# Kernel optimization log

Hardware: AMD Instinct MI355X
Metric: run time of the kernel (lower is better)

## Reference

```python
import jax, jax.numpy as jnp
import numpy as np

B = 2048          # batch of tree nodes
C = 256           # num_classes (GRU input size)
HS = 512          # h_size
H2 = 2 * HS       # GRU hidden size
D = 8             # max_output_degree


def setup_inputs() -> dict:
    key = jax.random.key(0)
    ks = jax.random.split(key, 12)
    s_ih = 1.0 / np.sqrt(C)
    s_h = 1.0 / np.sqrt(H2)
    return {
        "parent_output_label": jax.random.uniform(ks[0], (B, C), dtype=jnp.float32),
        "parent_h": jax.random.normal(ks[1], (B, HS), dtype=jnp.float32),
        "encoding": jax.random.normal(ks[2], (B, HS), dtype=jnp.float32),
        # stacked GRUCell params over the D output-degree slots
        "W_ih": jax.random.uniform(ks[3], (D, 3 * H2, C), jnp.float32, -s_ih, s_ih),
        "W_hh": jax.random.uniform(ks[4], (D, 3 * H2, H2), jnp.float32, -s_h, s_h),
        "b_ih": jax.random.uniform(ks[5], (D, 3 * H2), jnp.float32, -s_h, s_h),
        "b_hh": jax.random.uniform(ks[6], (D, 3 * H2), jnp.float32, -s_h, s_h),
        # stacked linear_probs (2h -> 1) and linear_hiddens (2h -> h)
        "W_p": jax.random.uniform(ks[7], (D, H2), jnp.float32, -s_h, s_h),
        "b_p": jax.random.uniform(ks[8], (D,), jnp.float32, -s_h, s_h),
        "W_h": jax.random.uniform(ks[9], (D, HS, H2), jnp.float32, -s_h, s_h),
        "b_h": jax.random.uniform(ks[10], (D, HS), jnp.float32, -s_h, s_h),
    }


def _compute_state_probs(x, h0, W_ih, W_hh, b_ih, b_hh, W_p, b_p, W_h, b_h):
    # x: [B, C], h0: [B, H2]. All D GRUCells fused into batched einsums.
    gi = jnp.einsum("bc,dgc->bdg", x, W_ih) + b_ih[None]        # [B, D, 3*H2]
    gh = jnp.einsum("bh,dgh->bdg", h0, W_hh) + b_hh[None]       # [B, D, 3*H2]
    i_r, i_z, i_n = jnp.split(gi, 3, axis=-1)
    h_r, h_z, h_n = jnp.split(gh, 3, axis=-1)
    r = jax.nn.sigmoid(i_r + h_r)
    z = jax.nn.sigmoid(i_z + h_z)
    n = jnp.tanh(i_n + r * h_n)
    hn = (1.0 - z) * n + z * h0[:, None, :]                      # [B, D, H2]
    probs = jax.nn.sigmoid(jnp.einsum("bdh,dh->bd", hn, W_p) + b_p[None])  # [B, D]
    hc = jnp.einsum("bdh,dkh->bdk", hn, W_h) + b_h[None]         # [B, D, HS]
    h = jnp.tanh(jnp.sum(hc, axis=1))                            # activ over summed slot hiddens
    return h, probs


def reference(parent_output_label, parent_h, encoding,
              W_ih, W_hh, b_ih, b_hh, W_p, b_p, W_h, b_h):
    h0 = jnp.concatenate([parent_h, encoding], axis=1)           # [B, 2*h_size]
    return _compute_state_probs(parent_output_label, h0,
                                W_ih, W_hh, b_ih, b_hh, W_p, b_p, W_h, b_h)
```

## Files before the change

### kernel.cpp

```cpp
#include <hip/hip_runtime.h>


#define B_   2048
#define C_   256
#define HS_  512
#define H2_  1024
#define G3_  3072
#define D_   8
#define NG_  24576

typedef __attribute__((ext_vector_type(8))) short bfrag;
typedef __attribute__((ext_vector_type(4))) float f32x4;

static __device__ __forceinline__ unsigned short f2bf(float f) {
  unsigned u = __float_as_uint(f);
  u = (u + 0x7FFFu + ((u >> 16) & 1u)) >> 16;
  return (unsigned short)u;
}
static __device__ __forceinline__ float bf2f(unsigned short s) {
  return __uint_as_float(((unsigned)s) << 16);
}
static __device__ __forceinline__ float fast_sigmoid(float x) {
  return 1.f / (1.f + __expf(-x));
}
static __device__ __forceinline__ float fast_tanh(float x) {
  return 1.f - 2.f / (__expf(2.f * x) + 1.f);
}

__device__ __forceinline__ void load16(const void* g, void* l) {
  __builtin_amdgcn_global_load_lds((const __attribute__((address_space(1))) void*)g,
                                   (__attribute__((address_space(3))) void*)l,
                                   16, 0, 0);
}

__global__ __launch_bounds__(256) void pack_kernel(
    const float* __restrict__ x, const float* __restrict__ ph,
    const float* __restrict__ enc, const float* __restrict__ Wih,
    const float* __restrict__ Whh, const float* __restrict__ Wh,
    unsigned short* __restrict__ A1, unsigned short* __restrict__ A2,
    unsigned short* __restrict__ BWih, unsigned short* __restrict__ BWhh,
    unsigned short* __restrict__ BWh)
{
  const long long total4 = 38273024LL / 4;
  const long long stride = (long long)gridDim.x * blockDim.x;
  for (long long i = (long long)blockIdx.x * blockDim.x + threadIdx.x;
       i < total4; i += stride) {
    long long o = i * 4;
    float4 v;
    unsigned short* dst;
    if (o < 524288) {
      v = *(const float4*)(x + o);
      dst = A1 + o;
    } else if (o < 2621440) {
      long long rel = o - 524288;
      int b = (int)(rel >> 10), c = (int)(rel & 1023);
      const float* src = (c < 512) ? (ph + b * 512 + c) : (enc + b * 512 + (c - 512));
      v = *(const float4*)src;
      dst = A2 + rel;
    } else if (o < 8912896) {
      long long rel = o - 2621440;
      v = *(const float4*)(Wih + rel);
      dst = BWih + rel;
    } else if (o < 34078720) {
      long long rel = o - 8912896;
      v = *(const float4*)(Whh + rel);
      dst = BWhh + rel;
    } else {
      long long rel = o - 34078720;
      int kk = (int)(rel >> 13);
      int r2 = (int)(rel & 8191);
      int d = r2 >> 10, hh = r2 & 1023;
      v = *(const float4*)(Wh + ((long long)d * 524288 + kk * 1024 + hh));
      dst = BWh + rel;
    }
    ushort4 w;
    w.x = f2bf(v.x); w.y = f2bf(v.y); w.z = f2bf(v.z); w.w = f2bf(v.w);
    *(ushort4*)dst = w;
  }
}

__global__ __launch_bounds__(512, 2) void gemm256(
    const unsigned short* __restrict__ A, const unsigned short* __restrict__ Bt,
    unsigned short* __restrict__ out, int M, int N, int K)
{
  extern __shared__ char lds[];
  const int t = threadIdx.x;
  const int wave = t >> 6, lane = t & 63;
  const int wr = wave >> 2, wc = wave & 3;
  const int la = lane & 15, ls = lane >> 4;

  const int gridY = M >> 8;
  const int q8 = gridDim.x >> 3;
  const int orig = blockIdx.x;
  const int swz = (orig & 7) * q8 + (orig >> 3);
  const int by = swz % gridY;
  const int bx = swz / gridY;
  const int brow = by << 8, bcol = bx << 8;
  const int nT = K >> 6;

  const int srr = t >> 3;
  const int ssc = ((t & 7) ^ ((t >> 3) & 7)) << 3;

  auto stageA = [&](int kt, int buf, int hf) {
    const unsigned short* src = A + (size_t)(brow + hf * 128 + srr) * K + kt * 64 + ssc;
    char* dst = lds + buf * 32768 + hf * 16384 + t * 16;
    load16(src, dst);
    load16(src + (size_t)64 * K, dst + 8192);
  };
  auto stageB = [&](int kt, int buf, int hf) {
    const unsigned short* src = Bt + (size_t)(bcol + hf * 128 + srr) * K + kt * 64 + ssc;
    char* dst = lds + 65536 + buf * 32768 + hf * 16384 + t * 16;
    load16(src, dst);
    load16(src + (size_t)64 * K, dst + 8192);
  };

  const int t1 = (nT > 1) ? 1 : 0;
  stageA(0, 0, 0); stageA(0, 0, 1);
  stageB(0, 0, 0); stageB(0, 0, 1);
  stageA(t1, 1, 0); stageA(t1, 1, 1);
  asm volatile("s_waitcnt vmcnt(4)" ::: "memory");
  __builtin_amdgcn_s_barrier();

  f32x4 acc[8][4];
#pragma unroll
  for (int m = 0; m < 8; ++m)
#pragma unroll
    for (int n = 0; n < 4; ++n) acc[m][n] = (f32x4){0.f, 0.f, 0.f, 0.f};

  const int sw = (la & 7) << 4;
  const int c0 = (ls << 4) ^ sw;

  for (int kt = 0; kt < nT; ++kt) {
    const int buf = kt & 1;
    const int kt1 = (kt + 1 < nT) ? kt + 1 : nT - 1;
    const int kt2 = (kt + 2 < nT) ? kt + 2 : nT - 1;
    const char* ab = lds + buf * 32768 + wr * 16384;
    const char* bb = lds + 65536 + buf * 32768 + (wc >> 1) * 16384;
    const int brb = (wc & 1) * 64;
    bfrag a0[8], a1[8], b0[4], b1[4];

#pragma unroll
    for (int m = 0; m < 8; ++m)
      a0[m] = *(const bfrag*)(ab + (m * 16 + la) * 128 + c0);
#pragma unroll
    for (int n = 0; n < 4; ++n)
      b0[n] = *(const bfrag*)(bb + (brb + n * 16 + la) * 128 + c0);
    stageB(kt1, buf ^ 1, 0);
    __builtin_amdgcn_s_barrier();
    __builtin_amdgcn_s_setprio(1);
#pragma unroll
    for (int m = 0; m < 4; ++m)
#pragma unroll
      for (int n = 0; n < 4; ++n)
        acc[m][n] = __builtin_amdgcn_mfma_f32_16x16x32_bf16(a0[m], b0[n], acc[m][n], 0, 0, 0);
    __builtin_amdgcn_s_setprio(0);
    __builtin_amdgcn_s_barrier();

#pragma unroll
    for (int m = 0; m < 8; ++m)
      a1[m] = *(const bfrag*)(ab + (m * 16 + la) * 128 + (c0 ^ 64));
    stageB(kt1, buf ^ 1, 1);
    __builtin_amdgcn_s_barrier();
    __builtin_amdgcn_s_setprio(1);
#pragma unroll
    for (int m = 4; m < 8; ++m)
#pragma unroll
      for (int n = 0; n < 4; ++n)
        acc[m][n] = __builtin_amdgcn_mfma_f32_16x16x32_bf16(a0[m], b0[n], acc[m][n], 0, 0, 0);
    __builtin_amdgcn_s_setprio(0);
    asm volatile("s_waitcnt lgkmcnt(0)" ::: "memory");
    __builtin_amdgcn_s_barrier();

#pragma unroll
    for (int n = 0; n < 4; ++n)
      b1[n] = *(const bfrag*)(bb + (brb + n * 16 + la) * 128 + (c0 ^ 64));
    stageA(kt2, buf, 0);
    __builtin_amdgcn_s_barrier();
    __builtin_amdgcn_s_setprio(1);
#pragma unroll
    for (int m = 0; m < 4; ++m)
#pragma unroll
      for (int n = 0; n < 4; ++n)
        acc[m][n] = __builtin_amdgcn_mfma_f32_16x16x32_bf16(a1[m], b1[n], acc[m][n], 0, 0, 0);
    __builtin_amdgcn_s_setprio(0);
    __builtin_amdgcn_s_barrier();

    stageA(kt2, buf, 1);
    __builtin_amdgcn_s_barrier();
    __builtin_amdgcn_s_setprio(1);
#pragma unroll
    for (int m = 4; m < 8; ++m)
#pragma unroll
      for (int n = 0; n < 4; ++n)
        acc[m][n] = __builtin_amdgcn_mfma_f32_16x16x32_bf16(a1[m], b1[n], acc[m][n], 0, 0, 0);
    __builtin_amdgcn_s_setprio(0);
    asm volatile("s_waitcnt vmcnt(4)" ::: "memory");
    __builtin_amdgcn_s_barrier();
  }

  const int orow = brow + wr * 128 + ls * 4;
  const int ocol = bcol + wc * 64 + la;
#pragma unroll
  for (int m = 0; m < 8; ++m)
#pragma unroll
    for (int n = 0; n < 4; ++n)
#pragma unroll
      for (int r = 0; r < 4; ++r)
        out[(size_t)(orow + m * 16 + r) * N + (ocol + n * 16)] = f2bf(acc[m][n][r]);
}

__global__ __launch_bounds__(256) void gemm_bt(
    const unsigned short* __restrict__ A, const unsigned short* __restrict__ Bt,
    void* __restrict__ out, int M, int N, int K, int kPerSlice, int outF32)
{
  __shared__ unsigned short sA[128 * 32];
  __shared__ unsigned short sB[128 * 32];
  const int t = threadIdx.x;
  const int wave = t >> 6, lane = t & 63;
  const int wr = wave >> 1, wc = wave & 1;
  const int brow = blockIdx.y << 7;
  const int bcol = blockIdx.x << 7;
  const int kOff = blockIdx.z * kPerSlice;

  f32x4 acc[4][4];
#pragma unroll
  for (int m = 0; m < 4; m++)
#pragma unroll
    for (int n = 0; n < 4; n++) acc[m][n] = (f32x4){0.f, 0.f, 0.f, 0.f};

  const int srow = t >> 2;
  const int scol = (t & 3) << 3;
  const unsigned short* aSrc = A + (size_t)(brow + srow) * K + kOff + scol;
  const unsigned short* bSrc = Bt + (size_t)(bcol + srow) * K + kOff + scol;
  const size_t rowStep = (size_t)64 * K;
  unsigned short* dA0 = sA + wave * 512;
  unsigned short* dA1 = sA + 2048 + wave * 512;
  unsigned short* dB0 = sB + wave * 512;
  unsigned short* dB1 = sB + 2048 + wave * 512;

  const int la = lane & 15;
  const int lk = (lane >> 4) << 3;
  const int kSteps = kPerSlice >> 5;

  for (int ks = 0; ks < kSteps; ++ks) {
    load16(aSrc, dA0);
    load16(aSrc + rowStep, dA1);
    load16(bSrc, dB0);
    load16(bSrc + rowStep, dB1);
    aSrc += 32; bSrc += 32;
    __syncthreads();
    bfrag aF[4], bF[4];
#pragma unroll
    for (int m = 0; m < 4; m++)
      aF[m] = *(const bfrag*)&sA[(wr * 64 + m * 16 + la) * 32 + lk];
#pragma unroll
    for (int n = 0; n < 4; n++)
      bF[n] = *(const bfrag*)&sB[(wc * 64 + n * 16 + la) * 32 + lk];
#pragma unroll
    for (int m = 0; m < 4; m++)
#pragma unroll
      for (int n = 0; n < 4; n++)
        acc[m][n] = __builtin_amdgcn_mfma_f32_16x16x32_bf16(aF[m], bF[n], acc[m][n], 0, 0, 0);
    __syncthreads();
  }

  const int orow = brow + wr * 64 + (lane >> 4) * 4;
  const int ocol = bcol + wc * 64 + la;
  if (outF32) {
    float* o = (float*)out + (size_t)blockIdx.z * ((size_t)M * N);
#pragma unroll
    for (int m = 0; m < 4; m++) {
      const int rb = orow + m * 16;
#pragma unroll
      for (int n = 0; n < 4; n++) {
        const int cb = ocol + n * 16;
#pragma unroll
        for (int r = 0; r < 4; r++)
          o[(size_t)(rb + r) * N + cb] = acc[m][n][r];
      }
    }
  } else {
    unsigned short* o = (unsigned short*)out;
#pragma unroll
    for (int m = 0; m < 4; m++) {
      const int rb = orow + m * 16;
#pragma unroll
      for (int n = 0; n < 4; n++) {
        const int cb = ocol + n * 16;
#pragma unroll
        for (int r = 0; r < 4; r++)
          o[(size_t)(rb + r) * N + cb] = f2bf(acc[m][n][r]);
      }
    }
  }
}

__global__ __launch_bounds__(256) void gru_pointwise(
    const unsigned short* __restrict__ Gi, const unsigned short* __restrict__ Gh,
    const float* __restrict__ b_ih, const float* __restrict__ b_hh,
    const float* __restrict__ ph, const float* __restrict__ enc,
    const float* __restrict__ W_p, const float* __restrict__ b_p,
    unsigned short* __restrict__ hn, float* __restrict__ probs)
{
  const int bd = blockIdx.x;
  const int b = bd >> 3, d = bd & 7;
  const int t = threadIdx.x;
  const size_t gbase = (size_t)b * NG_ + (size_t)d * G3_;
  const int bbase = d * G3_;
  float partial = 0.f;
#pragma unroll
  for (int i = 0; i < 4; ++i) {
    const int h = t + (i << 8);
    float ir  = bf2f(Gi[gbase + h])        + b_ih[bbase + h];
    float iz  = bf2f(Gi[gbase + 1024 + h]) + b_ih[bbase + 1024 + h];
    float inn = bf2f(Gi[gbase + 2048 + h]) + b_ih[bbase + 2048 + h];
    float hr  = bf2f(Gh[gbase + h])        + b_hh[bbase + h];
    float hz  = bf2f(Gh[gbase + 1024 + h]) + b_hh[bbase + 1024 + h];
    float hnn = bf2f(Gh[gbase + 2048 + h]) + b_hh[bbase + 2048 + h];
    float r = fast_sigmoid(ir + hr);
    float z = fast_sigmoid(iz + hz);
    float nn = fast_tanh(inn + r * hnn);
    float h0 = (h < 512) ? ph[b * 512 + h] : enc[b * 512 + h - 512];
    float hv = (1.f - z) * nn + z * h0;
    hn[(size_t)b * 8192 + d * 1024 + h] = f2bf(hv);
    partial += hv * W_p[d * 1024 + h];
  }
  __shared__ float red[256];
  red[t] = partial;
  __syncthreads();
  for (int s = 128; s > 0; s >>= 1) {
    if (t < s) red[t] += red[t + s];
    __syncthreads();
  }
  if (t == 0) probs[bd] = fast_sigmoid(red[0] + b_p[d]);
}

__global__ __launch_bounds__(256) void reduce_h_kernel(
    const float* __restrict__ part, const float* __restrict__ b_h,
    float* __restrict__ hout)
{
  const int idx = blockIdx.x * 256 + threadIdx.x;
  const int kk = idx & 511;
  float s = 0.f;
#pragma unroll
  for (int sl = 0; sl < 8; ++sl) s += part[(size_t)sl * 1048576 + idx];
  float bias = 0.f;
#pragma unroll
  for (int d = 0; d < 8; ++d) bias += b_h[d * 512 + kk];
  hout[idx] = fast_tanh(s + bias);
}

extern "C" void kernel_launch(void* const* d_in, const int* in_sizes, int n_in,
                              void* d_out, int out_size, void* d_ws, size_t ws_size,
                              hipStream_t stream) {
  const float* x   = (const float*)d_in[0];
  const float* ph  = (const float*)d_in[1];
  const float* enc = (const float*)d_in[2];
  const float* Wih = (const float*)d_in[3];
  const float* Whh = (const float*)d_in[4];
  const float* bih = (const float*)d_in[5];
  const float* bhh = (const float*)d_in[6];
  const float* Wp  = (const float*)d_in[7];
  const float* bp  = (const float*)d_in[8];
  const float* Wh  = (const float*)d_in[9];
  const float* bh  = (const float*)d_in[10];
  float* out = (float*)d_out;
  char* ws = (char*)d_ws;

  unsigned short* A1   = (unsigned short*)(ws + 0);
  unsigned short* A2   = (unsigned short*)(ws + 1048576);
  unsigned short* BWih = (unsigned short*)(ws + 5242880);
  unsigned short* BWhh = (unsigned short*)(ws + 17825792);
  unsigned short* BWh  = (unsigned short*)(ws + 68157440);
  unsigned short* Gi   = (unsigned short*)(ws + 76546048);
  unsigned short* Gh   = (unsigned short*)(ws + 177209344);
  unsigned short* hn   = (unsigned short*)(ws + 277872640);
  float*          part = (float*)(ws + 311427072);

  hipFuncSetAttribute((const void*)gemm256,
                      hipFuncAttributeMaxDynamicSharedMemorySize, 131072);

  pack_kernel<<<2048, 256, 0, stream>>>(x, ph, enc, Wih, Whh, Wh,
                                        A1, A2, BWih, BWhh, BWh);

  const int nwg = (NG_ / 256) * (B_ / 256);
  gemm256<<<nwg, 512, 131072, stream>>>(A1, BWih, Gi, B_, NG_, C_);
  gemm256<<<nwg, 512, 131072, stream>>>(A2, BWhh, Gh, B_, NG_, H2_);

  gru_pointwise<<<B_ * D_, 256, 0, stream>>>(Gi, Gh, bih, bhh, ph, enc, Wp, bp,
                                             hn, out + 1048576);

  dim3 g3(HS_ / 128, B_ / 128, 8);
  gemm_bt<<<g3, 256, 0, stream>>>(hn, BWh, part, B_, HS_, 8192, 1024, 1);

  reduce_h_kernel<<<4096, 256, 0, stream>>>(part, bh, out);
}
```

Measured before the change: 308.0 us.

## Fuse input and hidden GRU GEMMs into one K-concatenated GEMM

Packs x, parent_h and encoding into one [B,1280] activation and W_ih|W_hh into one [24576,1280] weight, then runs a single GEMM whose accumulator holds gi+gh for the r and z gates. For n-gate tiles, the input-only partial is written out after the first four K-tiles (K=256) and the accumulator is reset, so the r*h_n term stays correct. This removes one GEMM launch and the full Gi intermediate write/read, and the pointwise kernel reads fewer bytes using vectorized loads. The GEMM pipeline is reordered so that A and B tiles are both prefetched two stages ahead, and there is an extra mid-loop store branch on n-gate tiles.

```diff
diff --git a/kernel.cpp b/kernel.cpp
--- a/kernel.cpp
+++ b/kernel.cpp
@@ -8,6 +8,7 @@
 #define G3_  3072
 #define D_   8
 #define NG_  24576
+#define KF_  1280
 
 typedef __attribute__((ext_vector_type(8))) short bfrag;
 typedef __attribute__((ext_vector_type(4))) float f32x4;
@@ -37,8 +38,7 @@
     const float* __restrict__ x, const float* __restrict__ ph,
     const float* __restrict__ enc, const float* __restrict__ Wih,
     const float* __restrict__ Whh, const float* __restrict__ Wh,
-    unsigned short* __restrict__ A1, unsigned short* __restrict__ A2,
-    unsigned short* __restrict__ BWih, unsigned short* __restrict__ BWhh,
+    unsigned short* __restrict__ A, unsigned short* __restrict__ Bf,
     unsigned short* __restrict__ BWh)
 {
   const long long total4 = 38273024LL / 4;
@@ -46,57 +46,54 @@
   for (long long i = (long long)blockIdx.x * blockDim.x + threadIdx.x;
        i < total4; i += stride) {
     long long o = i * 4;
-    float4 v;
+    const float* src;
     unsigned short* dst;
-    if (o < 524288) {
-      v = *(const float4*)(x + o);
-      dst = A1 + o;
-    } else if (o < 2621440) {
-      long long rel = o - 524288;
-      int b = (int)(rel >> 10), c = (int)(rel & 1023);
-      const float* src = (c < 512) ? (ph + b * 512 + c) : (enc + b * 512 + (c - 512));
-      v = *(const float4*)src;
-      dst = A2 + rel;
-    } else if (o < 8912896) {
-      long long rel = o - 2621440;
-      v = *(const float4*)(Wih + rel);
-      dst = BWih + rel;
+    if (o < 2621440) {
+      unsigned rel = (unsigned)o;
+      unsigned b = rel / 1280u, c = rel % 1280u;
+      if (c < 256) src = x + (size_t)b * 256 + c;
+      else if (c < 768) src = ph + (size_t)b * 512 + (c - 256);
+      else src = enc + (size_t)b * 512 + (c - 768);
+      dst = A + rel;
     } else if (o < 34078720) {
-      long long rel = o - 8912896;
-      v = *(const float4*)(Whh + rel);
-      dst = BWhh + rel;
+      unsigned rel = (unsigned)(o - 2621440);
+      unsigned g = rel / 1280u, c = rel % 1280u;
+      src = (c < 256) ? (Wih + (size_t)g * 256 + c)
+                      : (Whh + (size_t)g * 1024 + (c - 256));
+      dst = Bf + rel;
     } else {
-      long long rel = o - 34078720;
-      int kk = (int)(rel >> 13);
-      int r2 = (int)(rel & 8191);
-      int d = r2 >> 10, hh = r2 & 1023;
-      v = *(const float4*)(Wh + ((long long)d * 524288 + kk * 1024 + hh));
+      unsigned rel = (unsigned)(o - 34078720);
+      unsigned kk = rel >> 13;
+      unsigned r2 = rel & 8191;
+      unsigned d = r2 >> 10, hh = r2 & 1023;
+      src = Wh + ((size_t)d * 524288 + (size_t)kk * 1024 + hh);
       dst = BWh + rel;
     }
+    float4 v = *(const float4*)src;
     ushort4 w;
     w.x = f2bf(v.x); w.y = f2bf(v.y); w.z = f2bf(v.z); w.w = f2bf(v.w);
     *(ushort4*)dst = w;
   }
 }
 
-__global__ __launch_bounds__(512, 2) void gemm256(
+__global__ __launch_bounds__(512, 2) void gemm_fused(
     const unsigned short* __restrict__ A, const unsigned short* __restrict__ Bt,
-    unsigned short* __restrict__ out, int M, int N, int K)
+    unsigned short* __restrict__ Gsum, unsigned short* __restrict__ In)
 {
   extern __shared__ char lds[];
+  const int K = KF_, N = NG_;
   const int t = threadIdx.x;
   const int wave = t >> 6, lane = t & 63;
   const int wr = wave >> 2, wc = wave & 3;
   const int la = lane & 15, ls = lane >> 4;
 
-  const int gridY = M >> 8;
   const int q8 = gridDim.x >> 3;
   const int orig = blockIdx.x;
   const int swz = (orig & 7) * q8 + (orig >> 3);
-  const int by = swz % gridY;
-  const int bx = swz / gridY;
-  const int brow = by << 8, bcol = bx << 8;
+  const int brow = (swz & 7) << 8;
+  const int bcol = (swz >> 3) << 8;
   const int nT = K >> 6;
+  const bool isN = ((bcol % G3_) >= 2048);
 
   const int srr = t >> 3;
   const int ssc = ((t & 7) ^ ((t >> 3) & 7)) << 3;
@@ -114,11 +111,9 @@
     load16(src + (size_t)64 * K, dst + 8192);
   };
 
-  const int t1 = (nT > 1) ? 1 : 0;
-  stageA(0, 0, 0); stageA(0, 0, 1);
-  stageB(0, 0, 0); stageB(0, 0, 1);
-  stageA(t1, 1, 0); stageA(t1, 1, 1);
-  asm volatile("s_waitcnt vmcnt(4)" ::: "memory");
+  stageA(0, 0, 0); stageA(0, 0, 1); stageB(0, 0, 0); stageB(0, 0, 1);
+  stageA(1, 1, 0); stageA(1, 1, 1); stageB(1, 1, 0); stageB(1, 1, 1);
+  asm volatile("s_waitcnt vmcnt(8)" ::: "memory");
   __builtin_amdgcn_s_barrier();
 
   f32x4 acc[8][4];
@@ -130,9 +125,12 @@
   const int sw = (la & 7) << 4;
   const int c0 = (ls << 4) ^ sw;
 
+  const int orow = brow + wr * 128 + ls * 4;
+  const int ocol = bcol + wc * 64 + la;
+
+#pragma unroll 1
   for (int kt = 0; kt < nT; ++kt) {
     const int buf = kt & 1;
-    const int kt1 = (kt + 1 < nT) ? kt + 1 : nT - 1;
     const int kt2 = (kt + 2 < nT) ? kt + 2 : nT - 1;
     const char* ab = lds + buf * 32768 + wr * 16384;
     const char* bb = lds + 65536 + buf * 32768 + (wc >> 1) * 16384;
@@ -145,7 +143,6 @@
 #pragma unroll
     for (int n = 0; n < 4; ++n)
       b0[n] = *(const bfrag*)(bb + (brb + n * 16 + la) * 128 + c0);
-    stageB(kt1, buf ^ 1, 0);
     __builtin_amdgcn_s_barrier();
     __builtin_amdgcn_s_setprio(1);
 #pragma unroll
@@ -159,7 +156,6 @@
 #pragma unroll
     for (int m = 0; m < 8; ++m)
       a1[m] = *(const bfrag*)(ab + (m * 16 + la) * 128 + (c0 ^ 64));
-    stageB(kt1, buf ^ 1, 1);
     __builtin_amdgcn_s_barrier();
     __builtin_amdgcn_s_setprio(1);
 #pragma unroll
@@ -175,6 +171,7 @@
     for (int n = 0; n < 4; ++n)
       b1[n] = *(const bfrag*)(bb + (brb + n * 16 + la) * 128 + (c0 ^ 64));
     stageA(kt2, buf, 0);
+    stageA(kt2, buf, 1);
     __builtin_amdgcn_s_barrier();
     __builtin_amdgcn_s_setprio(1);
 #pragma unroll
@@ -183,9 +180,11 @@
       for (int n = 0; n < 4; ++n)
         acc[m][n] = __builtin_amdgcn_mfma_f32_16x16x32_bf16(a1[m], b1[n], acc[m][n], 0, 0, 0);
     __builtin_amdgcn_s_setprio(0);
-    __builtin_amdgcn_s_barrier();
-
-    stageA(kt2, buf, 1);
+    asm volatile("s_waitcnt lgkmcnt(0)" ::: "memory");
+    __builtin_amdgcn_s_barrier();
+
+    stageB(kt2, buf, 0);
+    stageB(kt2, buf, 1);
     __builtin_amdgcn_s_barrier();
     __builtin_amdgcn_s_setprio(1);
 #pragma unroll
@@ -194,24 +193,37 @@
       for (int n = 0; n < 4; ++n)
         acc[m][n] = __builtin_amdgcn_mfma_f32_16x16x32_bf16(a1[m], b1[n], acc[m][n], 0, 0, 0);
     __builtin_amdgcn_s_setprio(0);
-    asm volatile("s_waitcnt vmcnt(4)" ::: "memory");
-    __builtin_amdgcn_s_barrier();
-  }
-
-  const int orow = brow + wr * 128 + ls * 4;
-  const int ocol = bcol + wc * 64 + la;
+    asm volatile("s_waitcnt vmcnt(8)" ::: "memory");
+    __builtin_amdgcn_s_barrier();
+
+    if (isN && kt == 3) {
+      const int d = bcol / G3_;
+      const int jb = (bcol % G3_) - 2048 + wc * 64;
+#pragma unroll
+      for (int m = 0; m < 8; ++m)
+#pragma unroll
+        for (int n = 0; n < 4; ++n) {
+#pragma unroll
+          for (int r = 0; r < 4; ++r)
+            In[(size_t)(orow + m * 16 + r) * 8192 + d * 1024 + jb + n * 16 + la]
+                = f2bf(acc[m][n][r]);
+          acc[m][n] = (f32x4){0.f, 0.f, 0.f, 0.f};
+        }
+    }
+  }
+
 #pragma unroll
   for (int m = 0; m < 8; ++m)
 #pragma unroll
     for (int n = 0; n < 4; ++n)
 #pragma unroll
       for (int r = 0; r < 4; ++r)
-        out[(size_t)(orow + m * 16 + r) * N + (ocol + n * 16)] = f2bf(acc[m][n][r]);
+        Gsum[(size_t)(orow + m * 16 + r) * N + (ocol + n * 16)] = f2bf(acc[m][n][r]);
 }
 
 __global__ __launch_bounds__(256) void gemm_bt(
     const unsigned short* __restrict__ A, const unsigned short* __restrict__ Bt,
-    void* __restrict__ out, int M, int N, int K, int kPerSlice, int outF32)
+    float* __restrict__ out, int M, int N, int K, int kPerSlice)
 {
   __shared__ unsigned short sA[128 * 32];
   __shared__ unsigned short sB[128 * 32];
@@ -266,37 +278,22 @@
 
   const int orow = brow + wr * 64 + (lane >> 4) * 4;
   const int ocol = bcol + wc * 64 + la;
-  if (outF32) {
-    float* o = (float*)out + (size_t)blockIdx.z * ((size_t)M * N);
-#pragma unroll
-    for (int m = 0; m < 4; m++) {
-      const int rb = orow + m * 16;
-#pragma unroll
-      for (int n = 0; n < 4; n++) {
-        const int cb = ocol + n * 16;
-#pragma unroll
-        for (int r = 0; r < 4; r++)
-          o[(size_t)(rb + r) * N + cb] = acc[m][n][r];
-      }
+  float* o = out + (size_t)blockIdx.z * ((size_t)M * N);
+#pragma unroll
+  for (int m = 0; m < 4; m++) {
+    const int rb = orow + m * 16;
+#pragma unroll
+    for (int n = 0; n < 4; n++) {
+      const int cb = ocol + n * 16;
+#pragma unroll
+      for (int r = 0; r < 4; r++)
+        o[(size_t)(rb + r) * N + cb] = acc[m][n][r];
     }
-  } else {
-    unsigned short* o = (unsigned short*)out;
-#pragma unroll
-    for (int m = 0; m < 4; m++) {
-      const int rb = orow + m * 16;
-#pragma unroll
-      for (int n = 0; n < 4; n++) {
-        const int cb = ocol + n * 16;
-#pragma unroll
-        for (int r = 0; r < 4; r++)
-          o[(size_t)(rb + r) * N + cb] = f2bf(acc[m][n][r]);
-      }
-    }
   }
 }
 
 __global__ __launch_bounds__(256) void gru_pointwise(
-    const unsigned short* __restrict__ Gi, const unsigned short* __restrict__ Gh,
+    const unsigned short* __restrict__ Gsum, const unsigned short* __restrict__ In,
     const float* __restrict__ b_ih, const float* __restrict__ b_hh,
     const float* __restrict__ ph, const float* __restrict__ enc,
     const float* __restrict__ W_p, const float* __restrict__ b_p,
@@ -306,24 +303,31 @@
   const int b = bd >> 3, d = bd & 7;
   const int t = threadIdx.x;
   const size_t gbase = (size_t)b * NG_ + (size_t)d * G3_;
-  const int bbase = d * G3_;
+  const size_t ibase = (size_t)b * 8192 + (size_t)d * 1024;
+  const int bb = d * G3_;
   float partial = 0.f;
 #pragma unroll
-  for (int i = 0; i < 4; ++i) {
-    const int h = t + (i << 8);
-    float ir  = bf2f(Gi[gbase + h])        + b_ih[bbase + h];
-    float iz  = bf2f(Gi[gbase + 1024 + h]) + b_ih[bbase + 1024 + h];
-    float inn = bf2f(Gi[gbase + 2048 + h]) + b_ih[bbase + 2048 + h];
-    float hr  = bf2f(Gh[gbase + h])        + b_hh[bbase + h];
-    float hz  = bf2f(Gh[gbase + 1024 + h]) + b_hh[bbase + 1024 + h];
-    float hnn = bf2f(Gh[gbase + 2048 + h]) + b_hh[bbase + 2048 + h];
-    float r = fast_sigmoid(ir + hr);
-    float z = fast_sigmoid(iz + hz);
-    float nn = fast_tanh(inn + r * hnn);
-    float h0 = (h < 512) ? ph[b * 512 + h] : enc[b * 512 + h - 512];
-    float hv = (1.f - z) * nn + z * h0;
-    hn[(size_t)b * 8192 + d * 1024 + h] = f2bf(hv);
-    partial += hv * W_p[d * 1024 + h];
+  for (int i = 0; i < 2; ++i) {
+    const int h = 2 * t + (i << 9);
+    ushort2 gr = *(const ushort2*)(Gsum + gbase + h);
+    ushort2 gz = *(const ushort2*)(Gsum + gbase + 1024 + h);
+    ushort2 gn = *(const ushort2*)(Gsum + gbase + 2048 + h);
+    ushort2 gi = *(const ushort2*)(In + ibase + h);
+    ushort2 hv2;
+#pragma unroll
+    for (int j = 0; j < 2; ++j) {
+      const int hj = h + j;
+      float r = fast_sigmoid(bf2f(j ? gr.y : gr.x) + b_ih[bb + hj] + b_hh[bb + hj]);
+      float z = fast_sigmoid(bf2f(j ? gz.y : gz.x) + b_ih[bb + 1024 + hj] + b_hh[bb + 1024 + hj]);
+      float inn = bf2f(j ? gi.y : gi.x) + b_ih[bb + 2048 + hj];
+      float hnn = bf2f(j ? gn.y : gn.x) + b_hh[bb + 2048 + hj];
+      float nn = fast_tanh(inn + r * hnn);
+      float h0 = (hj < 512) ? ph[b * 512 + hj] : enc[b * 512 + hj - 512];
+      float hv = (1.f - z) * nn + z * h0;
+      if (j) hv2.y = f2bf(hv); else hv2.x = f2bf(hv);
+      partial += hv * W_p[d * 1024 + hj];
+    }
+    *(ushort2*)(hn + ibase + h) = hv2;
   }
   __shared__ float red[256];
   red[t] = partial;
@@ -367,31 +371,27 @@
   float* out = (float*)d_out;
   char* ws = (char*)d_ws;
 
-  unsigned short* A1   = (unsigned short*)(ws + 0);
-  unsigned short* A2   = (unsigned short*)(ws + 1048576);
-  unsigned short* BWih = (unsigned short*)(ws + 5242880);
-  unsigned short* BWhh = (unsigned short*)(ws + 17825792);
+  unsigned short* A    = (unsigned short*)(ws + 0);
+  unsigned short* Bf   = (unsigned short*)(ws + 5242880);
   unsigned short* BWh  = (unsigned short*)(ws + 68157440);
-  unsigned short* Gi   = (unsigned short*)(ws + 76546048);
-  unsigned short* Gh   = (unsigned short*)(ws + 177209344);
-  unsigned short* hn   = (unsigned short*)(ws + 277872640);
-  float*          part = (float*)(ws + 311427072);
-
-  hipFuncSetAttribute((const void*)gemm256,
+  unsigned short* Gsum = (unsigned short*)(ws + 76546048);
+  unsigned short* In   = (unsigned short*)(ws + 177209344);
+  unsigned short* hn   = (unsigned short*)(ws + 210763776);
+  float*          part = (float*)(ws + 244318208);
+
+  hipFuncSetAttribute((const void*)gemm_fused,
                       hipFuncAttributeMaxDynamicSharedMemorySize, 131072);
 
-  pack_kernel<<<2048, 256, 0, stream>>>(x, ph, enc, Wih, Whh, Wh,
-                                        A1, A2, BWih, BWhh, BWh);
+  pack_kernel<<<2048, 256, 0, stream>>>(x, ph, enc, Wih, Whh, Wh, A, Bf, BWh);
 
   const int nwg = (NG_ / 256) * (B_ / 256);
-  gemm256<<<nwg, 512, 131072, stream>>>(A1, BWih, Gi, B_, NG_, C_);
-  gemm256<<<nwg, 512, 131072, stream>>>(A2, BWhh, Gh, B_, NG_, H2_);
-
-  gru_pointwise<<<B_ * D_, 256, 0, stream>>>(Gi, Gh, bih, bhh, ph, enc, Wp, bp,
+  gemm_fused<<<nwg, 512, 131072, stream>>>(A, Bf, Gsum, In);
+
+  gru_pointwise<<<B_ * D_, 256, 0, stream>>>(Gsum, In, bih, bhh, ph, enc, Wp, bp,
                                              hn, out + 1048576);
 
   dim3 g3(HS_ / 128, B_ / 128, 8);
-  gemm_bt<<<g3, 256, 0, stream>>>(hn, BWh, part, B_, HS_, 8192, 1024, 1);
+  gemm_bt<<<g3, 256, 0, stream>>>(hn, BWh, part, B_, HS_, 8192, 1024);
 
   reduce_h_kernel<<<4096, 256, 0, stream>>>(part, bh, out);
 }
```

Result: slower. 380.7 us (+23.6%).
